# Kernel tuning notes

Hardware: AMD Instinct MI355X
Metric: run time of the kernel (lower is better)

Reference implementation:

```python
import jax, jax.numpy as jnp
import numpy as np

B, S, D, F, E = 4, 4096, 1024, 2048, 8


def setup_inputs() -> dict:
    key = jax.random.key(0)
    ks = jax.random.split(key, 8)
    x = jax.random.normal(ks[0], (B, S, D), dtype=jnp.float32)
    # router (nn.Linear(d_model, num_experts))
    Wr = jax.random.normal(ks[1], (D, E), dtype=jnp.float32) * 0.02
    br = jnp.zeros((E,), dtype=jnp.float32)
    # stacked per-expert MLP params: Linear(D,F) -> GELU -> Linear(F,D)
    W1 = jax.random.normal(ks[2], (E, D, F), dtype=jnp.float32) * (1.0 / np.sqrt(D))
    b1 = jnp.zeros((E, F), dtype=jnp.float32)
    W2 = jax.random.normal(ks[3], (E, F, D), dtype=jnp.float32) * (1.0 / np.sqrt(F))
    b2 = jnp.zeros((E, D), dtype=jnp.float32)
    return {"x": x, "Wr": Wr, "br": br, "W1": W1, "b1": b1, "W2": W2, "b2": b2}


def reference(x, Wr, br, W1, b1, W2, b2):
    # router: softmax over experts, top-1 selection
    logits = jnp.einsum("bsd,de->bse", x, Wr) + br          # [B,S,E]
    probs = jax.nn.softmax(logits, axis=-1)
    expert_weights = jnp.max(probs, axis=-1)                  # [B,S]
    expert_indices = jnp.argmax(probs, axis=-1)               # [B,S]

    num_experts = W1.shape[0]
    out = jnp.zeros_like(x)
    # loop over the small fixed set of experts (structurally distinct weights)
    for e in range(num_experts):
        h = jax.nn.gelu(jnp.einsum("bsd,df->bsf", x, W1[e]) + b1[e], approximate=False)
        y = jnp.einsum("bsf,fd->bsd", h, W2[e]) + b2[e]
        out = jnp.where((expert_indices == e)[..., None], y, out)

    return out * expert_weights[..., None]
```

## Files before the change

### kernel.cpp

```cpp
#include <hip/hip_runtime.h>
#include <hip/hip_bf16.h>


typedef __attribute__((ext_vector_type(8))) short short8;
typedef __attribute__((ext_vector_type(4))) float f32x4;

struct __align__(8) us4 { unsigned short x, y, z, w; };

__device__ __forceinline__ void gload16(const void* g, void* l) {
  __builtin_amdgcn_global_load_lds(
      (const __attribute__((address_space(1))) unsigned int*)g,
      (__attribute__((address_space(3))) unsigned int*)l, 16, 0, 0);
}

__device__ __forceinline__ unsigned short f2b(float f) {
  union { float f; unsigned u; } v; v.f = f;
  unsigned r = v.u + 0x7FFFu + ((v.u >> 16) & 1u);
  return (unsigned short)(r >> 16);
}

__global__ __launch_bounds__(256) void router_logits(
    const float* __restrict__ x, const float* __restrict__ Wr,
    const float* __restrict__ br, float* __restrict__ wts,
    int* __restrict__ eidx, unsigned short* __restrict__ xb)
{
  const int lane = threadIdx.x & 63;
  const int wid  = threadIdx.x >> 6;
  const int t = blockIdx.x * 4 + wid;

  const float4* x4 = (const float4*)(x + (size_t)t * 1024);
  float acc[8];
#pragma unroll
  for (int e = 0; e < 8; ++e) acc[e] = 0.f;
#pragma unroll
  for (int i = 0; i < 4; ++i) {
    float4 v = x4[lane + 64 * i];
    const int d = (lane + 64 * i) * 4;
    const float* wr = Wr + (size_t)d * 8;
    float xs[4] = {v.x, v.y, v.z, v.w};
    us4 o;
    o.x = f2b(v.x); o.y = f2b(v.y); o.z = f2b(v.z); o.w = f2b(v.w);
    *(us4*)(xb + (size_t)t * 1024 + (size_t)(lane + 64 * i) * 4) = o;
#pragma unroll
    for (int j = 0; j < 4; ++j) {
      float4 w0 = *(const float4*)(wr + j * 8);
      float4 w1 = *(const float4*)(wr + j * 8 + 4);
      acc[0] += xs[j] * w0.x; acc[1] += xs[j] * w0.y;
      acc[2] += xs[j] * w0.z; acc[3] += xs[j] * w0.w;
      acc[4] += xs[j] * w1.x; acc[5] += xs[j] * w1.y;
      acc[6] += xs[j] * w1.z; acc[7] += xs[j] * w1.w;
    }
  }
#pragma unroll
  for (int e = 0; e < 8; ++e) {
    float v = acc[e];
#pragma unroll
    for (int m = 32; m; m >>= 1) v += __shfl_xor(v, m, 64);
    acc[e] = v;
  }
  if (lane == 0) {
    float lg[8];
#pragma unroll
    for (int e = 0; e < 8; ++e) lg[e] = acc[e] + br[e];
    float mx = lg[0]; int bi = 0;
#pragma unroll
    for (int e = 1; e < 8; ++e) if (lg[e] > mx) { mx = lg[e]; bi = e; }
    float s = 0.f;
#pragma unroll
    for (int e = 0; e < 8; ++e) s += expf(lg[e] - mx);
    wts[t]  = 1.0f / s;
    eidx[t] = bi;
  }
}

__global__ __launch_bounds__(256) void bucketize(
    const int* __restrict__ eidx, int* __restrict__ cnt, int* __restrict__ list)
{
  __shared__ int lcnt[8], base[8];
  const int tid = threadIdx.x;
  if (tid < 8) lcnt[tid] = 0;
  __syncthreads();
  const int t = blockIdx.x * 256 + tid;
  const int e = eidx[t];
  const int lpos = atomicAdd(&lcnt[e], 1);
  __syncthreads();
  if (tid < 8) base[tid] = atomicAdd(&cnt[tid], lcnt[tid]);
  __syncthreads();
  list[e * 16384 + base[e] + lpos] = t;
}

__global__ __launch_bounds__(256) void transpose_cvt(
    const float* __restrict__ W, unsigned short* __restrict__ Wt, int K, int N)
{
  __shared__ float tl[64][65];
  const int e = blockIdx.z;
  const float* Wp = W + (size_t)e * K * N;
  unsigned short* Wtp = Wt + (size_t)e * K * N;
  const int k0 = blockIdx.y * 64, n0 = blockIdx.x * 64;
  const int r = threadIdx.x >> 4, c4 = (threadIdx.x & 15) * 4;
#pragma unroll
  for (int i = 0; i < 4; ++i) {
    float4 v = *(const float4*)(Wp + (size_t)(k0 + r + i * 16) * N + n0 + c4);
    tl[r + i * 16][c4 + 0] = v.x; tl[r + i * 16][c4 + 1] = v.y;
    tl[r + i * 16][c4 + 2] = v.z; tl[r + i * 16][c4 + 3] = v.w;
  }
  __syncthreads();
#pragma unroll
  for (int i = 0; i < 4; ++i) {
    const int n = r + i * 16;
    us4 o;
    o.x = f2b(tl[c4 + 0][n]); o.y = f2b(tl[c4 + 1][n]);
    o.z = f2b(tl[c4 + 2][n]); o.w = f2b(tl[c4 + 3][n]);
    *(us4*)(Wtp + (size_t)(n0 + n) * K + k0 + c4) = o;
  }
}

template <int K, int N, int EPI, int LOGNB>
__global__ __launch_bounds__(512, 2) void gemm_moe8(
    const unsigned short* __restrict__ A,
    const unsigned short* __restrict__ Bt,
    const float* __restrict__ bias,
    const int* __restrict__ cnt, const int* __restrict__ list,
    const float* __restrict__ wts, void* __restrict__ outp)
{
  constexpr int NT = K / 64;
  constexpr int NB = 1 << LOGNB;
  extern __shared__ char lds[];
  int*   tok_s = (int*)(lds + 131072);
  float* wt_s  = (float*)(lds + 132096);

  const int q = gridDim.x >> 3;
  const int p = ((int)blockIdx.x & 7) * q + ((int)blockIdx.x >> 3);
  int e = -1, pre = 0, cnte = 0, loc = p;
#pragma unroll
  for (int i = 0; i < 8; ++i) {
    const int c = cnt[i];
    const int bl = ((c + 255) >> 8) << LOGNB;
    if (e < 0) {
      if (loc < bl) { e = i; cnte = c; }
      else { loc -= bl; pre += c; }
    }
  }
  if (e < 0) return;
  const int row0 = (loc >> LOGNB) << 8;
  const int n0   = (loc & (NB - 1)) << 8;

  const int tid = threadIdx.x;
  const int lane = tid & 63, wid = tid >> 6;
  const int wr = wid >> 2, wc = wid & 3;
  const int l15 = lane & 15, hi = lane >> 4;

  if (tid < 256) {
    const int s = row0 + tid;
    if (s < cnte) {
      const int t = list[e * 16384 + s];
      tok_s[tid] = t;
      wt_s[tid]  = (EPI == 2) ? wts[t] : 0.f;
    } else { tok_s[tid] = 0; wt_s[tid] = 0.f; }
  }
  __syncthreads();

  const int r8 = lane >> 3;
  const int ch = (lane & 7) ^ r8;
  const unsigned short* aP[4];
  const unsigned short* bP[4];
#pragma unroll
  for (int k2 = 0; k2 < 4; ++k2) {
    const int row = wid * 8 + r8 + k2 * 64;
    if (EPI == 1) aP[k2] = A + (size_t)tok_s[row] * K + ch * 8;
    else          aP[k2] = A + (size_t)min(pre + row0 + row, 16383) * K + ch * 8;
    bP[k2] = Bt + ((size_t)e * N + n0 + row) * K + ch * 8;
  }

  const int sl0 = ((hi ^ (l15 & 7)) << 4);
  const int sl1 = (((4 + hi) ^ (l15 & 7)) << 4);
  const char* aR0 = lds + (size_t)(wr * 128 + l15) * 128 + sl0;
  const char* aR1 = lds + (size_t)(wr * 128 + l15) * 128 + sl1;
  const char* bR0 = lds + 65536 + (size_t)(wc * 64 + l15) * 128 + sl0;
  const char* bR1 = lds + 65536 + (size_t)(wc * 64 + l15) * 128 + sl1;

  f32x4 acc[8][4];
#pragma unroll
  for (int m = 0; m < 8; ++m)
#pragma unroll
    for (int n = 0; n < 4; ++n) acc[m][n] = (f32x4){0.f, 0.f, 0.f, 0.f};

#define STG_A(BUF, T) do { _Pragma("unroll") \
    for (int k2 = 0; k2 < 4; ++k2) \
      gload16(aP[k2] + (size_t)(T) * 64, lds + (BUF) * 32768 + wid * 1024 + k2 * 8192); \
  } while (0)
#define STG_B(BUF, T) do { _Pragma("unroll") \
    for (int k2 = 0; k2 < 4; ++k2) \
      gload16(bP[k2] + (size_t)(T) * 64, lds + 65536 + (BUF) * 32768 + wid * 1024 + k2 * 8192); \
  } while (0)
#define BARF() do { __builtin_amdgcn_s_barrier(); asm volatile("" ::: "memory"); } while (0)

  STG_A(0, 0); STG_B(0, 0);
  asm volatile("s_waitcnt vmcnt(0)" ::: "memory");
  BARF();

  short8 aF[8], bA[4], bB[4];
#pragma unroll 1
  for (int T = 0; T < NT; ++T) {
    const int buf = T & 1, bufn = buf ^ 1;
    const int Ts = (T + 1 < NT) ? T + 1 : NT - 1;
    const char* a0 = aR0 + buf * 32768;
    const char* a1 = aR1 + buf * 32768;
    const char* b0 = bR0 + buf * 32768;
    const char* b1 = bR1 + buf * 32768;

#pragma unroll
    for (int m = 0; m < 4; ++m) {
      aF[2 * m]     = *(const short8*)(a0 + m * 2048);
      aF[2 * m + 1] = *(const short8*)(a1 + m * 2048);
    }
#pragma unroll
    for (int n = 0; n < 2; ++n) {
      bA[2 * n]     = *(const short8*)(b0 + n * 2048);
      bA[2 * n + 1] = *(const short8*)(b1 + n * 2048);
    }
    STG_A(bufn, Ts);
    BARF();
    __builtin_amdgcn_s_setprio(1);
#pragma unroll
    for (int m = 0; m < 4; ++m)
#pragma unroll
      for (int n = 0; n < 2; ++n) {
        acc[m][n] = __builtin_amdgcn_mfma_f32_16x16x32_bf16(aF[2 * m], bA[2 * n], acc[m][n], 0, 0, 0);
        acc[m][n] = __builtin_amdgcn_mfma_f32_16x16x32_bf16(aF[2 * m + 1], bA[2 * n + 1], acc[m][n], 0, 0, 0);
      }
    __builtin_amdgcn_s_setprio(0);
    BARF();

#pragma unroll
    for (int n = 0; n < 2; ++n) {
      bB[2 * n]     = *(const short8*)(b0 + (2 + n) * 2048);
      bB[2 * n + 1] = *(const short8*)(b1 + (2 + n) * 2048);
    }
    STG_B(bufn, Ts);
    BARF();
    __builtin_amdgcn_s_setprio(1);
#pragma unroll
    for (int m = 0; m < 4; ++m)
#pragma unroll
      for (int n = 0; n < 2; ++n) {
        acc[m][2 + n] = __builtin_amdgcn_mfma_f32_16x16x32_bf16(aF[2 * m], bB[2 * n], acc[m][2 + n], 0, 0, 0);
        acc[m][2 + n] = __builtin_amdgcn_mfma_f32_16x16x32_bf16(aF[2 * m + 1], bB[2 * n + 1], acc[m][2 + n], 0, 0, 0);
      }
    __builtin_amdgcn_s_setprio(0);
    BARF();

#pragma unroll
    for (int m = 0; m < 4; ++m) {
      aF[2 * m]     = *(const short8*)(a0 + (4 + m) * 2048);
      aF[2 * m + 1] = *(const short8*)(a1 + (4 + m) * 2048);
    }
    BARF();
    __builtin_amdgcn_s_setprio(1);
#pragma unroll
    for (int m = 0; m < 4; ++m)
#pragma unroll
      for (int n = 0; n < 2; ++n) {
        acc[4 + m][2 + n] = __builtin_amdgcn_mfma_f32_16x16x32_bf16(aF[2 * m], bB[2 * n], acc[4 + m][2 + n], 0, 0, 0);
        acc[4 + m][2 + n] = __builtin_amdgcn_mfma_f32_16x16x32_bf16(aF[2 * m + 1], bB[2 * n + 1], acc[4 + m][2 + n], 0, 0, 0);
      }
    __builtin_amdgcn_s_setprio(0);
    BARF();

    asm volatile("s_waitcnt vmcnt(0)" ::: "memory");
    BARF();
    __builtin_amdgcn_s_setprio(1);
#pragma unroll
    for (int m = 0; m < 4; ++m)
#pragma unroll
      for (int n = 0; n < 2; ++n) {
        acc[4 + m][n] = __builtin_amdgcn_mfma_f32_16x16x32_bf16(aF[2 * m], bA[2 * n], acc[4 + m][n], 0, 0, 0);
        acc[4 + m][n] = __builtin_amdgcn_mfma_f32_16x16x32_bf16(aF[2 * m + 1], bA[2 * n + 1], acc[4 + m][n], 0, 0, 0);
      }
    __builtin_amdgcn_s_setprio(0);
    BARF();
  }
#undef STG_A
#undef STG_B
#undef BARF

  const int cRow0 = wr * 128 + (hi << 2);
  const int cColB = n0 + wc * 64 + l15;
  float bv[4];
#pragma unroll
  for (int nf = 0; nf < 4; ++nf) bv[nf] = bias[e * N + cColB + nf * 16];

  if (EPI == 1) {
    unsigned short* H = (unsigned short*)outp;
#pragma unroll
    for (int m = 0; m < 8; ++m)
#pragma unroll
      for (int r = 0; r < 4; ++r) {
        const int sl = cRow0 + m * 16 + r;
        if (row0 + sl < cnte) {
          const size_t rp = (size_t)(pre + row0 + sl) * N + cColB;
#pragma unroll
          for (int nf = 0; nf < 4; ++nf) {
            float v = acc[m][nf][r] + bv[nf];
            float u = 1.5957691216f * v * (1.0f + 0.044715f * v * v);
            float ex = __expf(u);
            float th = 1.0f - 2.0f / (ex + 1.0f);
            v = 0.5f * v * (1.0f + th);
            H[rp + nf * 16] = f2b(v);
          }
        }
      }
  } else {
    float* O = (float*)outp;
#pragma unroll
    for (int m = 0; m < 8; ++m)
#pragma unroll
      for (int r = 0; r < 4; ++r) {
        const int sl = cRow0 + m * 16 + r;
        if (row0 + sl < cnte) {
          const size_t rp = (size_t)tok_s[sl] * N + cColB;
          const float w = wt_s[sl];
#pragma unroll
          for (int nf = 0; nf < 4; ++nf)
            O[rp + nf * 16] = (acc[m][nf][r] + bv[nf]) * w;
        }
      }
  }
}

extern "C" void kernel_launch(void* const* d_in, const int* in_sizes, int n_in,
                              void* d_out, int out_size, void* d_ws, size_t ws_size,
                              hipStream_t stream) {
  const float* x  = (const float*)d_in[0];
  const float* Wr = (const float*)d_in[1];
  const float* br = (const float*)d_in[2];
  const float* W1 = (const float*)d_in[3];
  const float* b1 = (const float*)d_in[4];
  const float* W2 = (const float*)d_in[5];
  const float* b2 = (const float*)d_in[6];

  char* ws = (char*)d_ws;
  int*   cnt  = (int*)ws;
  float* wts  = (float*)(ws + 256);
  int*   eidx = (int*)(ws + 256 + 64 * 1024);
  int*   list = (int*)(ws + 256 + 128 * 1024);
  unsigned short* xb  = (unsigned short*)(ws + 1024 * 1024);
  unsigned short* w1t = xb  + (size_t)16384 * 1024;
  unsigned short* w2t = w1t + (size_t)8 * 2048 * 1024;
  unsigned short* h   = w2t + (size_t)8 * 1024 * 2048;

  constexpr int LDS_BYTES = 133120;
  hipFuncSetAttribute((const void*)gemm_moe8<1024, 2048, 1, 3>,
                      hipFuncAttributeMaxDynamicSharedMemorySize, LDS_BYTES);
  hipFuncSetAttribute((const void*)gemm_moe8<2048, 1024, 2, 2>,
                      hipFuncAttributeMaxDynamicSharedMemorySize, LDS_BYTES);

  hipMemsetAsync(cnt, 0, 32, stream);
  router_logits<<<dim3(4096), 256, 0, stream>>>(x, Wr, br, wts, eidx, xb);
  bucketize<<<dim3(64), 256, 0, stream>>>(eidx, cnt, list);
  transpose_cvt<<<dim3(32, 16, 8), 256, 0, stream>>>(W1, w1t, 1024, 2048);
  transpose_cvt<<<dim3(16, 32, 8), 256, 0, stream>>>(W2, w2t, 2048, 1024);
  gemm_moe8<1024, 2048, 1, 3><<<dim3(71 * 8), 512, LDS_BYTES, stream>>>(
      xb, w1t, b1, cnt, list, wts, (void*)h);
  gemm_moe8<2048, 1024, 2, 2><<<dim3(72 * 4), 512, LDS_BYTES, stream>>>(
      h, w2t, b2, cnt, list, wts, d_out);
}
```

Measured before the change: 360.3 us.

## Deepen GEMM K-loop prefetch to two tiles ahead with split half-tile loads

Restructures the MFMA K-loop so global-to-LDS loads run two K-tiles ahead instead of one. Each tile's A/B load is split into halves issued at different phases, and waits use partial vmcnt counts instead of draining to zero. Several barriers are removed or replaced with lgkmcnt waits, which cuts synchronisation per iteration and hides more memory latency. The risk is correctness of buffer reuse, because the current buffer is overwritten with tile T+2 while other waves may still read it, and the partial vmcnt counting is fragile.

```diff
diff --git a/kernel.cpp b/kernel.cpp
--- a/kernel.cpp
+++ b/kernel.cpp
@@ -185,25 +185,32 @@
 #pragma unroll
     for (int n = 0; n < 4; ++n) acc[m][n] = (f32x4){0.f, 0.f, 0.f, 0.f};
 
-#define STG_A(BUF, T) do { _Pragma("unroll") \
-    for (int k2 = 0; k2 < 4; ++k2) \
-      gload16(aP[k2] + (size_t)(T) * 64, lds + (BUF) * 32768 + wid * 1024 + k2 * 8192); \
+#define STG_AH(BUF, T, H) do { _Pragma("unroll") \
+    for (int k2 = 2 * (H); k2 < 2 * (H) + 2; ++k2) \
+      gload16(aP[k2] + (size_t)(T) * 64, lds + (BUF) * 32768 + k2 * 8192 + (wid << 10)); \
   } while (0)
-#define STG_B(BUF, T) do { _Pragma("unroll") \
-    for (int k2 = 0; k2 < 4; ++k2) \
-      gload16(bP[k2] + (size_t)(T) * 64, lds + 65536 + (BUF) * 32768 + wid * 1024 + k2 * 8192); \
+#define STG_BH(BUF, T, H) do { _Pragma("unroll") \
+    for (int k2 = 2 * (H); k2 < 2 * (H) + 2; ++k2) \
+      gload16(bP[k2] + (size_t)(T) * 64, lds + 65536 + (BUF) * 32768 + k2 * 8192 + (wid << 10)); \
   } while (0)
-#define BARF() do { __builtin_amdgcn_s_barrier(); asm volatile("" ::: "memory"); } while (0)
-
-  STG_A(0, 0); STG_B(0, 0);
-  asm volatile("s_waitcnt vmcnt(0)" ::: "memory");
-  BARF();
+#define LGKM_BAR() do { \
+    asm volatile("s_waitcnt lgkmcnt(0)" ::: "memory"); \
+    __builtin_amdgcn_sched_barrier(0); \
+    __builtin_amdgcn_s_barrier(); \
+    asm volatile("" ::: "memory"); } while (0)
+
+  STG_BH(0, 0, 0); STG_AH(0, 0, 0); STG_AH(0, 0, 1); STG_BH(0, 0, 1);
+  STG_BH(1, 1, 0); STG_AH(1, 1, 0); STG_AH(1, 1, 1);
+  asm volatile("s_waitcnt vmcnt(6)" ::: "memory");
+  __builtin_amdgcn_s_barrier();
+  asm volatile("" ::: "memory");
 
   short8 aF[8], bA[4], bB[4];
 #pragma unroll 1
   for (int T = 0; T < NT; ++T) {
     const int buf = T & 1, bufn = buf ^ 1;
-    const int Ts = (T + 1 < NT) ? T + 1 : NT - 1;
+    const int Ts1 = (T + 1 < NT) ? T + 1 : NT - 1;
+    const int Ts2 = (T + 2 < NT) ? T + 2 : NT - 1;
     const char* a0 = aR0 + buf * 32768;
     const char* a1 = aR1 + buf * 32768;
     const char* b0 = bR0 + buf * 32768;
@@ -219,8 +226,8 @@
       bA[2 * n]     = *(const short8*)(b0 + n * 2048);
       bA[2 * n + 1] = *(const short8*)(b1 + n * 2048);
     }
-    STG_A(bufn, Ts);
-    BARF();
+    STG_BH(bufn, Ts1, 1);
+    LGKM_BAR();
     __builtin_amdgcn_s_setprio(1);
 #pragma unroll
     for (int m = 0; m < 4; ++m)
@@ -230,15 +237,13 @@
         acc[m][n] = __builtin_amdgcn_mfma_f32_16x16x32_bf16(aF[2 * m + 1], bA[2 * n + 1], acc[m][n], 0, 0, 0);
       }
     __builtin_amdgcn_s_setprio(0);
-    BARF();
 
 #pragma unroll
     for (int n = 0; n < 2; ++n) {
       bB[2 * n]     = *(const short8*)(b0 + (2 + n) * 2048);
       bB[2 * n + 1] = *(const short8*)(b1 + (2 + n) * 2048);
     }
-    STG_B(bufn, Ts);
-    BARF();
+    LGKM_BAR();
     __builtin_amdgcn_s_setprio(1);
 #pragma unroll
     for (int m = 0; m < 4; ++m)
@@ -248,14 +253,14 @@
         acc[m][2 + n] = __builtin_amdgcn_mfma_f32_16x16x32_bf16(aF[2 * m + 1], bB[2 * n + 1], acc[m][2 + n], 0, 0, 0);
       }
     __builtin_amdgcn_s_setprio(0);
-    BARF();
 
 #pragma unroll
     for (int m = 0; m < 4; ++m) {
       aF[2 * m]     = *(const short8*)(a0 + (4 + m) * 2048);
       aF[2 * m + 1] = *(const short8*)(a1 + (4 + m) * 2048);
     }
-    BARF();
+    STG_BH(buf, Ts2, 0);
+    LGKM_BAR();
     __builtin_amdgcn_s_setprio(1);
 #pragma unroll
     for (int m = 0; m < 4; ++m)
@@ -265,10 +270,12 @@
         acc[4 + m][2 + n] = __builtin_amdgcn_mfma_f32_16x16x32_bf16(aF[2 * m + 1], bB[2 * n + 1], acc[4 + m][2 + n], 0, 0, 0);
       }
     __builtin_amdgcn_s_setprio(0);
-    BARF();
-
-    asm volatile("s_waitcnt vmcnt(0)" ::: "memory");
-    BARF();
+
+    STG_AH(buf, Ts2, 0);
+    STG_AH(buf, Ts2, 1);
+    asm volatile("s_waitcnt vmcnt(6)" ::: "memory");
+    __builtin_amdgcn_s_barrier();
+    asm volatile("" ::: "memory");
     __builtin_amdgcn_s_setprio(1);
 #pragma unroll
     for (int m = 0; m < 4; ++m)
@@ -278,11 +285,11 @@
         acc[4 + m][n] = __builtin_amdgcn_mfma_f32_16x16x32_bf16(aF[2 * m + 1], bA[2 * n + 1], acc[4 + m][n], 0, 0, 0);
       }
     __builtin_amdgcn_s_setprio(0);
-    BARF();
-  }
-#undef STG_A
-#undef STG_B
-#undef BARF
+  }
+#undef STG_AH
+#undef STG_BH
+#undef LGKM_BAR
+  asm volatile("s_waitcnt vmcnt(0)" ::: "memory");
 
   const int cRow0 = wr * 128 + (hi << 2);
   const int cColB = n0 + wc * 64 + l15;
```

After: 345.0 us. 4.2% less time.
